# Optimization experiments

Measured on AMD Instinct MI355X. Metric: run time of the kernel, lower is better.

## Reference

```python
import jax, jax.numpy as jnp
import numpy as np
import math

PHI = (1.0 + math.sqrt(5.0)) / 2.0
B, S, E, H = 4, 1024, 1024, 16
D = E // H  # head_dim = 64


def setup_inputs() -> dict:
    key = jax.random.key(0)
    ks = jax.random.split(key, 16)
    w = 0.02  # stand-in for xavier(gain=1/phi); math is init-agnostic
    inp = {
        "query": jax.random.normal(ks[0], (B, S, E), jnp.float32),
        "key": jax.random.normal(ks[1], (B, S, E), jnp.float32),
        "value": jax.random.normal(ks[2], (B, S, E), jnp.float32),
        "consciousness_levels": jax.random.uniform(ks[3], (B, S), jnp.float32),
        # causal mask, broadcast over batch and heads
        "attn_mask": jnp.tril(jnp.ones((S, S), bool))[None, None],
        # projection weights stored [in, out] (torch Linear applies x @ W.T)
        "Wq": jax.random.normal(ks[4], (E, E), jnp.float32) * w,
        "bq": jnp.zeros((E,), jnp.float32),
        "Wk": jax.random.normal(ks[5], (E, E), jnp.float32) * w,
        "bk": jnp.zeros((E,), jnp.float32),
        "Wv": jax.random.normal(ks[6], (E, E), jnp.float32) * w,
        "bv": jnp.zeros((E,), jnp.float32),
        "Wo": jax.random.normal(ks[7], (E, E), jnp.float32) * w,
        "bo": jnp.zeros((E,), jnp.float32),
        "Wc": jax.random.normal(ks[8], (E, H), jnp.float32) * w,
        "bc": jnp.zeros((H,), jnp.float32),
        # phi_bias[h] = (h+1)/phi**(h+1), shape [H,1,1] as in _init_weights
        "phi_bias": jnp.array([(h + 1) / PHI ** (h + 1) for h in range(H)],
                               jnp.float32).reshape(H, 1, 1),
    }
    return inp


def reference(query, key, value, consciousness_levels, attn_mask,
              Wq, bq, Wk, bk, Wv, bv, Wo, bo, Wc, bc, phi_bias):
    # project and split heads: [B,S,E] -> [B,H,S,D]
    q = (query @ Wq + bq).reshape(B, S, H, D).transpose(0, 2, 1, 3)
    k = (key @ Wk + bk).reshape(B, S, H, D).transpose(0, 2, 1, 3)
    v = (value @ Wv + bv).reshape(B, S, H, D).transpose(0, 2, 1, 3)

    inv_scale = 1.0 / (math.sqrt(D) * math.sqrt(PHI))  # phi-scaled 1/sqrt(d)
    scores = jnp.einsum('bhqd,bhkd->bhqk', q, k) * inv_scale
    scores = scores + phi_bias[None]                   # per-head additive bias
    scores = jnp.where(attn_mask, scores, -jnp.inf)
    attn = jax.nn.softmax(scores, axis=-1)             # [B,H,S,S]

    # consciousness reweighting + second softmax (faithful to original)
    cw = jax.nn.softmax(query @ Wc + bc, axis=-1)      # [B,S,H]
    cw = cw.transpose(0, 2, 1)[..., None]              # [B,H,S,1]
    cb = consciousness_levels[:, None, :, None]        # [B,1,S,1]
    attn = jax.nn.softmax(attn * (1.0 + cb * cw), axis=-1)

    ctx = jnp.einsum('bhqk,bhkd->bhqd', attn, v)
    ctx = ctx.transpose(0, 2, 1, 3).reshape(B, S, E)
    out = ctx @ Wo + bo
    return out, attn
```

## Files before the change

kernel.cpp:

```cpp
#include <hip/hip_runtime.h>
#include <stdint.h>

#define B_ 4
#define S_ 1024
#define E_ 1024
#define H_ 16
#define D_ 64

typedef unsigned short u16;
typedef short s16x8 __attribute__((ext_vector_type(8)));
typedef unsigned short u16x8 __attribute__((ext_vector_type(8)));
typedef unsigned short u16x4 __attribute__((ext_vector_type(4)));
typedef unsigned short u16x2 __attribute__((ext_vector_type(2)));
typedef float f32x4 __attribute__((ext_vector_type(4)));

__device__ __forceinline__ u16 f2bf(float f) {
    union { float f; uint32_t i; } x; x.f = f;
    uint32_t r = (x.i + 0x7FFFu + ((x.i >> 16) & 1u)) >> 16;
    return (u16)r;
}

__device__ __forceinline__ float wave_sum(float v) {
    #pragma unroll
    for (int o = 32; o; o >>= 1) v += __shfl_xor(v, o);
    return v;
}

__device__ __forceinline__ void gload16(const u16* g, u16* l) {
    __builtin_amdgcn_global_load_lds(
        (const __attribute__((address_space(1))) void*)g,
        (__attribute__((address_space(3))) void*)l, 16, 0, 0);
}

template<int BM, int BN>
__device__ __forceinline__ void gemm_core(
    const u16* __restrict__ Ab, int lda,
    const u16* __restrict__ Bp, int ldb,
    int m0, int n0, int K,
    u16* As, u16* Bs, f32x4 (&acc)[BM / 32][BN / 32])
{
    constexpr int FM = BM / 32, FN = BN / 32;
    constexpr int ACH = BM / 64;
    constexpr int BCH = BN / 64;
    const int t = threadIdx.x, lane = t & 63, w = t >> 6;
    const int wr = w >> 1, wc = w & 1, al = lane & 15, aq = lane >> 4;

    for (int k0 = 0; k0 < K; k0 += 32) {
        #pragma unroll
        for (int i = 0; i < ACH; i++) {
            const int c = i * 256 + w * 64 + lane;
            gload16(Ab + (size_t)(m0 + (c >> 2)) * lda + k0 + (c & 3) * 8,
                    As + (size_t)(i * 256 + w * 64) * 8);
        }
        #pragma unroll
        for (int i = 0; i < BCH; i++) {
            const int c = i * 256 + w * 64 + lane;
            gload16(Bp + (size_t)(n0 + (c >> 2)) * ldb + k0 + (c & 3) * 8,
                    Bs + (size_t)(i * 256 + w * 64) * 8);
        }
        asm volatile("s_waitcnt vmcnt(0)" ::: "memory");
        __syncthreads();

        s16x8 af[FM], bf[FN];
        #pragma unroll
        for (int i = 0; i < FM; i++)
            af[i] = *(const s16x8*)(As + ((wr * FM + i) * 16 + al) * 32 + aq * 8);
        #pragma unroll
        for (int j = 0; j < FN; j++)
            bf[j] = *(const s16x8*)(Bs + ((wc * FN + j) * 16 + al) * 32 + aq * 8);
        #pragma unroll
        for (int i = 0; i < FM; i++)
            #pragma unroll
            for (int j = 0; j < FN; j++)
                acc[i][j] = __builtin_amdgcn_mfma_f32_16x16x32_bf16(af[i], bf[j], acc[i][j], 0, 0, 0);
        __syncthreads();
    }
}

__global__ __launch_bounds__(256, 3)
void gemm_qkv(const u16* __restrict__ qbf, const u16* __restrict__ kbf,
              const u16* __restrict__ vbf, const u16* __restrict__ wt,
              const float* __restrict__ bq, const float* __restrict__ bk,
              const float* __restrict__ bv,
              u16* __restrict__ q_ws, u16* __restrict__ k_ws,
              u16* __restrict__ vt_ws)
{
    __shared__ __attribute__((aligned(16))) u16 As[128 * 32];
    __shared__ __attribute__((aligned(16))) u16 Bs[128 * 32];
    const int z = blockIdx.z;
    const u16* Ab = (z == 0) ? qbf : (z == 1) ? kbf : vbf;
    const u16* Bp = wt + (size_t)z * E_ * E_;
    const float* bias = (z == 0) ? bq : (z == 1) ? bk : bv;
    u16* Cb = (z == 0) ? q_ws : (z == 1) ? k_ws : vt_ws;
    const int m0 = blockIdx.y * 128, n0 = blockIdx.x * 128;

    f32x4 acc[4][4];
    #pragma unroll
    for (int i = 0; i < 4; i++)
        #pragma unroll
        for (int j = 0; j < 4; j++)
            acc[i][j] = (f32x4){0.f, 0.f, 0.f, 0.f};

    gemm_core<128, 128>(Ab, E_, Bp, E_, m0, n0, E_, As, Bs, acc);

    const int t = threadIdx.x, lane = t & 63, w = t >> 6;
    const int wr = w >> 1, wc = w & 1, al = lane & 15, aq = lane >> 4;
    #pragma unroll
    for (int i = 0; i < 4; i++) {
        #pragma unroll
        for (int j = 0; j < 4; j++) {
            const int col = n0 + (wc * 4 + j) * 16 + al;
            const float bvv = bias[col];
            #pragma unroll
            for (int r = 0; r < 4; r++) {
                const int row = m0 + (wr * 4 + i) * 16 + aq * 4 + r;
                const float vv = acc[i][j][r] + bvv;
                const int b = row >> 10, s = row & 1023, h = col >> 6, d = col & 63;
                if (z < 2)
                    Cb[((size_t)((b * H_ + h) * S_ + s)) * D_ + d] = f2bf(vv);
                else
                    Cb[((size_t)((b * H_ + h) * D_ + d)) * S_ + s] = f2bf(vv);
            }
        }
    }
}

__global__ __launch_bounds__(256, 3)
void gemm_o(const u16* __restrict__ ctx, const u16* __restrict__ wt3,
            const float* __restrict__ bo, float* __restrict__ out)
{
    __shared__ __attribute__((aligned(16))) u16 As[128 * 32];
    __shared__ __attribute__((aligned(16))) u16 Bs[64 * 32];
    const int m0 = blockIdx.y * 128, n0 = blockIdx.x * 64;

    f32x4 acc[4][2];
    #pragma unroll
    for (int i = 0; i < 4; i++)
        #pragma unroll
        for (int j = 0; j < 2; j++)
            acc[i][j] = (f32x4){0.f, 0.f, 0.f, 0.f};

    gemm_core<128, 64>(ctx, E_, wt3, E_, m0, n0, E_, As, Bs, acc);

    const int t = threadIdx.x, lane = t & 63, w = t >> 6;
    const int wr = w >> 1, wc = w & 1, al = lane & 15, aq = lane >> 4;
    #pragma unroll
    for (int i = 0; i < 4; i++) {
        #pragma unroll
        for (int j = 0; j < 2; j++) {
            const int col = n0 + (wc * 2 + j) * 16 + al;
            const float bvv = bo[col];
            #pragma unroll
            for (int r = 0; r < 4; r++) {
                const int row = m0 + (wr * 4 + i) * 16 + aq * 4 + r;
                out[(size_t)row * E_ + col] = acc[i][j][r] + bvv;
            }
        }
    }
}

__device__ __forceinline__ void cvt8(const float* __restrict__ src,
                                     u16* __restrict__ dst, int i) {
    f32x4 a = *(const f32x4*)(src + (size_t)i * 8);
    f32x4 b = *(const f32x4*)(src + (size_t)i * 8 + 4);
    u16x8 o;
    o[0] = f2bf(a[0]); o[1] = f2bf(a[1]); o[2] = f2bf(a[2]); o[3] = f2bf(a[3]);
    o[4] = f2bf(b[0]); o[5] = f2bf(b[1]); o[6] = f2bf(b[2]); o[7] = f2bf(b[3]);
    *(u16x8*)(dst + (size_t)i * 8) = o;
}

__global__ __launch_bounds__(256)
void cvt3_k(const float* __restrict__ q, const float* __restrict__ k,
            const float* __restrict__ v, u16* __restrict__ oq,
            u16* __restrict__ ok, u16* __restrict__ ov)
{
    const int n = B_ * S_ * E_ / 8;
    for (int i = blockIdx.x * 256 + threadIdx.x; i < n; i += gridDim.x * 256) {
        cvt8(q, oq, i);
        cvt8(k, ok, i);
        cvt8(v, ov, i);
    }
}

__global__ __launch_bounds__(256)
void cons_k(const float* __restrict__ query, const float* __restrict__ Wc,
            const float* __restrict__ bc, const float* __restrict__ cl,
            float* __restrict__ mws)
{
    const int t = threadIdx.x, lane = t & 63, wave = t >> 6;
    const int r = blockIdx.x * 4 + wave;
    const float* qrow = query + (size_t)r * E_;
    float acc[H_];
    #pragma unroll
    for (int c = 0; c < H_; c++) acc[c] = 0.f;
    for (int e = lane; e < E_; e += 64) {
        float qv = qrow[e];
        const float* wp = Wc + e * H_;
        f32x4 w0 = *(const f32x4*)(wp);
        f32x4 w1 = *(const f32x4*)(wp + 4);
        f32x4 w2 = *(const f32x4*)(wp + 8);
        f32x4 w3 = *(const f32x4*)(wp + 12);
        #pragma unroll
        for (int c = 0; c < 4; c++) {
            acc[c]      += qv * w0[c];
            acc[4 + c]  += qv * w1[c];
            acc[8 + c]  += qv * w2[c];
            acc[12 + c] += qv * w3[c];
        }
    }
    #pragma unroll
    for (int c = 0; c < H_; c++) acc[c] = wave_sum(acc[c]);
    float mx = -3e38f;
    #pragma unroll
    for (int c = 0; c < H_; c++) { acc[c] += bc[c]; mx = fmaxf(mx, acc[c]); }
    float se = 0.f;
    #pragma unroll
    for (int c = 0; c < H_; c++) { acc[c] = __expf(acc[c] - mx); se += acc[c]; }
    if (lane < H_) {
        float mycw = 0.f;
        #pragma unroll
        for (int c = 0; c < H_; c++) if (lane == c) mycw = acc[c];
        mycw /= se;
        int b = r >> 10, s = r & 1023;
        float clv = cl[r];
        mws[((size_t)(b * H_ + lane)) * S_ + s] = 1.f + clv * mycw;
    }
}

#define LD_ 1028
__global__ __launch_bounds__(512, 4)
void attn_fused(const u16* __restrict__ q_ws, const u16* __restrict__ k_ws,
                const u16* __restrict__ vt_ws, const float* __restrict__ mws,
                float* __restrict__ attn_out, u16* __restrict__ ctx_ws,
                float alpha)
{
    __shared__ __attribute__((aligned(16))) float sc[16 * LD_];
    __shared__ float red[32 * 16];
    __shared__ float rowmax[16], scl1[16], invz[16];

    const int t = threadIdx.x, lane = t & 63, w = t >> 6;
    const int al = lane & 15, aq = lane >> 4;
    const int bh = blockIdx.y;
    const int q0 = blockIdx.x * 16;

    const u16* Qp = q_ws + ((size_t)bh * S_ + q0) * D_;
    const u16* Kp = k_ws + ((size_t)bh * S_ + w * 128) * D_;
    const u16* Vp = vt_ws + (size_t)bh * D_ * S_;

    s16x8 qf0 = *(const s16x8*)(Qp + (size_t)al * D_ + aq * 8);
    s16x8 qf1 = *(const s16x8*)(Qp + (size_t)al * D_ + 32 + aq * 8);
    #pragma unroll
    for (int mf = 0; mf < 8; mf++) {
        const u16* kr = Kp + (size_t)(mf * 16 + al) * D_ + aq * 8;
        s16x8 kf0 = *(const s16x8*)(kr);
        s16x8 kf1 = *(const s16x8*)(kr + 32);
        f32x4 a0 = (f32x4){0.f, 0.f, 0.f, 0.f};
        a0 = __builtin_amdgcn_mfma_f32_16x16x32_bf16(kf0, qf0, a0, 0, 0, 0);
        a0 = __builtin_amdgcn_mfma_f32_16x16x32_bf16(kf1, qf1, a0, 0, 0, 0);
        const int kc = w * 128 + mf * 16 + aq * 4;
        f32x4 o;
        #pragma unroll
        for (int j = 0; j < 4; j++) o[j] = a0[j] * alpha;
        *(f32x4*)(sc + (size_t)al * LD_ + kc) = o;
    }
    __syncthreads();

    const int row = t & 15, cg = t >> 4;
    const int q = q0 + row;
    float* rp = sc + (size_t)row * LD_ + cg * 4;

    f32x4 sv[8];
    float mx = -3e38f;
    #pragma unroll
    for (int k = 0; k < 8; k++) {
        sv[k] = *(const f32x4*)(rp + k * 128);
        const int cb = cg * 4 + k * 128;
        #pragma unroll
        for (int j = 0; j < 4; j++)
            if (cb + j <= q) mx = fmaxf(mx, sv[k][j]);
    }
    red[cg * 16 + row] = mx;
    __syncthreads();
    if (t < 16) {
        float m = red[t];
        #pragma unroll
        for (int c = 1; c < 32; c++) m = fmaxf(m, red[c * 16 + t]);
        rowmax[t] = m;
    }
    __syncthreads();

    const float mxr = rowmax[row];
    float s1 = 0.f;
    #pragma unroll
    for (int k = 0; k < 8; k++) {
        const int cb = cg * 4 + k * 128;
        #pragma unroll
        for (int j = 0; j < 4; j++) {
            float e = (cb + j <= q) ? __expf(sv[k][j] - mxr) : 0.f;
            sv[k][j] = e; s1 += e;
        }
    }
    red[cg * 16 + row] = s1;
    __syncthreads();
    if (t < 16) {
        float s = 0.f;
        #pragma unroll
        for (int c = 0; c < 32; c++) s += red[c * 16 + t];
        scl1[t] = mws[(size_t)bh * S_ + q0 + t] / s;
    }
    __syncthreads();

    const float sl = scl1[row];
    float s2 = 0.f;
    #pragma unroll
    for (int k = 0; k < 8; k++) {
        const int cb = cg * 4 + k * 128;
        f32x4 o;
        #pragma unroll
        for (int j = 0; j < 4; j++) {
            float e = (cb + j <= q) ? __expf(sv[k][j] * sl) : 1.f;
            o[j] = e; s2 += e;
        }
        *(f32x4*)(rp + k * 128) = o;
    }
    red[cg * 16 + row] = s2;
    __syncthreads();
    if (t < 16) {
        float s = 0.f;
        #pragma unroll
        for (int c = 0; c < 32; c++) s += red[c * 16 + t];
        invz[t] = 1.f / s;
    }
    __syncthreads();

    f32x4 pa[4];
    #pragma unroll
    for (int nf = 0; nf < 4; nf++) pa[nf] = (f32x4){0.f, 0.f, 0.f, 0.f};
    #pragma unroll
    for (int ks = 0; ks < 4; ks++) {
        const int kb = w * 128 + ks * 32;
        const float* ap = sc + (size_t)al * LD_ + kb + aq * 8;
        f32x4 x0 = *(const f32x4*)(ap);
        f32x4 x1 = *(const f32x4*)(ap + 4);
        s16x8 af;
        af[0] = (short)f2bf(x0[0]); af[1] = (short)f2bf(x0[1]);
        af[2] = (short)f2bf(x0[2]); af[3] = (short)f2bf(x0[3]);
        af[4] = (short)f2bf(x1[0]); af[5] = (short)f2bf(x1[1]);
        af[6] = (short)f2bf(x1[2]); af[7] = (short)f2bf(x1[3]);
        #pragma unroll
        for (int nf = 0; nf < 4; nf++) {
            s16x8 bfv = *(const s16x8*)(Vp + (size_t)(nf * 16 + al) * S_ + kb + aq * 8);
            pa[nf] = __builtin_amdgcn_mfma_f32_16x16x32_bf16(af, bfv, pa[nf], 0, 0, 0);
        }
    }

    float* ao = attn_out + (size_t)bh * S_ * S_ + (size_t)q0 * S_;
    #pragma unroll
    for (int rr = 0; rr < 2; rr++) {
        const int r2 = w * 2 + rr;
        const float iz = invz[r2];
        #pragma unroll
        for (int k2 = 0; k2 < 4; k2++) {
            f32x4 v = *(const f32x4*)(sc + (size_t)r2 * LD_ + k2 * 256 + lane * 4);
            f32x4 o;
            #pragma unroll
            for (int j = 0; j < 4; j++) o[j] = v[j] * iz;
            *(f32x4*)(ao + (size_t)r2 * S_ + k2 * 256 + lane * 4) = o;
        }
    }
    __syncthreads();

    {
        float* dp = sc + w * (64 * 20);
        #pragma unroll
        for (int nf = 0; nf < 4; nf++)
            *(f32x4*)(dp + (size_t)(nf * 16 + al) * 20 + aq * 4) = pa[nf];
    }
    __syncthreads();
    {
        const int r5 = t >> 5, d0 = (t & 31) * 2;
        const float iz = invz[r5];
        float o0 = 0.f, o1 = 0.f;
        #pragma unroll
        for (int ww = 0; ww < 8; ww++) {
            const float* rp5 = sc + ww * (64 * 20) + r5;
            o0 += rp5[(size_t)d0 * 20];
            o1 += rp5[(size_t)(d0 + 1) * 20];
        }
        const int b = bh >> 4, h = bh & 15;
        u16* cp = ctx_ws + ((size_t)(b * S_ + q0 + r5)) * E_ + h * 64 + d0;
        u16x2 ob;
        ob[0] = f2bf(o0 * iz);
        ob[1] = f2bf(o1 * iz);
        *(u16x2*)cp = ob;
    }
}

__global__ __launch_bounds__(256)
void transpose4_k(const float* __restrict__ W0, const float* __restrict__ W1,
                  const float* __restrict__ W2, const float* __restrict__ W3,
                  u16* __restrict__ out)
{
    __shared__ float tile[32][33];
    const int zz = blockIdx.z;
    const float* in = (zz == 0) ? W0 : (zz == 1) ? W1 : (zz == 2) ? W2 : W3;
    u16* o = out + (size_t)zz * E_ * E_;
    const int t = threadIdx.x;
    const int tx = t & 31, ty = t >> 5;
    const int bx = blockIdx.x * 32, by = blockIdx.y * 32;
    #pragma unroll
    for (int i = 0; i < 32; i += 8)
        tile[ty + i][tx] = in[(size_t)(by + ty + i) * E_ + bx + tx];
    __syncthreads();
    #pragma unroll
    for (int i = 0; i < 32; i += 8)
        o[(size_t)(bx + ty + i) * E_ + by + tx] = f2bf(tile[tx][ty + i]);
}

extern "C" void kernel_launch(void* const* d_in, const int* in_sizes, int n_in,
                              void* d_out, int out_size, void* d_ws, size_t ws_size,
                              hipStream_t stream)
{
    const float* query = (const float*)d_in[0];
    const float* key_  = (const float*)d_in[1];
    const float* value = (const float*)d_in[2];
    const float* cl    = (const float*)d_in[3];
    const float* Wq = (const float*)d_in[5];
    const float* bq = (const float*)d_in[6];
    const float* Wk = (const float*)d_in[7];
    const float* bk = (const float*)d_in[8];
    const float* Wv = (const float*)d_in[9];
    const float* bv = (const float*)d_in[10];
    const float* Wo = (const float*)d_in[11];
    const float* bo = (const float*)d_in[12];
    const float* Wc = (const float*)d_in[13];
    const float* bc = (const float*)d_in[14];

    float* out  = (float*)d_out;
    float* attn = out + (size_t)B_ * S_ * E_;

    u16* q_ws   = (u16*)d_ws;
    u16* k_ws   = q_ws  + (size_t)B_ * S_ * E_;
    u16* vt_ws  = k_ws  + (size_t)B_ * S_ * E_;
    u16* ctx_ws = vt_ws + (size_t)B_ * S_ * E_;
    u16* wt     = ctx_ws + (size_t)B_ * S_ * E_;
    float* mws  = (float*)(wt + (size_t)4 * E_ * E_);

    u16* qbf = (u16*)attn;
    u16* kbf = qbf + (size_t)B_ * S_ * E_;
    u16* vbf = kbf + (size_t)B_ * S_ * E_;

    const float inv_scale = 0.09826892502579689f;
    dim3 blk(256);

    transpose4_k<<<dim3(32, 32, 4), blk, 0, stream>>>(Wq, Wk, Wv, Wo, wt);

    cvt3_k<<<2048, blk, 0, stream>>>(query, key_, value, qbf, kbf, vbf);

    cons_k<<<B_ * S_ / 4, blk, 0, stream>>>(query, Wc, bc, cl, mws);

    gemm_qkv<<<dim3(8, 32, 3), blk, 0, stream>>>(
        qbf, kbf, vbf, wt, bq, bk, bv, q_ws, k_ws, vt_ws);

    attn_fused<<<dim3(S_ / 16, B_ * H_), dim3(512), 0, stream>>>(
        q_ws, k_ws, vt_ws, mws, attn, ctx_ws, inv_scale);

    gemm_o<<<dim3(16, 32, 1), blk, 0, stream>>>(
        ctx_ws, wt + (size_t)3 * E_ * E_, bo, out);
}
```

Baseline: 556.8 us.

## Keep attention scores in registers, stage bf16 probabilities, and swizzle block order

The attention kernel now applies the mask and exponentials straight on the MFMA accumulators and keeps them in registers, instead of round-tripping fp32 scores through a large LDS tile. Row sums use wave shuffles plus a small LDS reduction. The unnormalised probabilities go into LDS as bf16 for the PV MFMA, which shrinks shared memory to raise occupancy. The row-max pass is dropped, which risks overflow if scores get large. All three kernels also remap block indices so neighbouring blocks share operand tiles in cache, and the attn_out stores become narrower per-lane scalar writes.

```diff
diff --git a/kernel.cpp b/kernel.cpp
--- a/kernel.cpp
+++ b/kernel.cpp
@@ -87,12 +87,15 @@
 {
     __shared__ __attribute__((aligned(16))) u16 As[128 * 32];
     __shared__ __attribute__((aligned(16))) u16 Bs[128 * 32];
-    const int z = blockIdx.z;
+    const int flat = blockIdx.x + (blockIdx.y << 3) + (blockIdx.z << 8);
+    const int z = flat >> 8;
+    const int y = flat & 31;
+    const int x = (flat >> 5) & 7;
     const u16* Ab = (z == 0) ? qbf : (z == 1) ? kbf : vbf;
     const u16* Bp = wt + (size_t)z * E_ * E_;
     const float* bias = (z == 0) ? bq : (z == 1) ? bk : bv;
     u16* Cb = (z == 0) ? q_ws : (z == 1) ? k_ws : vt_ws;
-    const int m0 = blockIdx.y * 128, n0 = blockIdx.x * 128;
+    const int m0 = y * 128, n0 = x * 128;
 
     f32x4 acc[4][4];
     #pragma unroll
@@ -131,7 +134,10 @@
 {
     __shared__ __attribute__((aligned(16))) u16 As[128 * 32];
     __shared__ __attribute__((aligned(16))) u16 Bs[64 * 32];
-    const int m0 = blockIdx.y * 128, n0 = blockIdx.x * 64;
+    const int flat = blockIdx.x + (blockIdx.y << 4);
+    const int y = flat & 31;
+    const int x = flat >> 5;
+    const int m0 = y * 128, n0 = x * 64;
 
     f32x4 acc[4][2];
     #pragma unroll
@@ -227,109 +233,114 @@
     }
 }
 
-#define LD_ 1028
+#define LDP 1048
 __global__ __launch_bounds__(512, 4)
 void attn_fused(const u16* __restrict__ q_ws, const u16* __restrict__ k_ws,
                 const u16* __restrict__ vt_ws, const float* __restrict__ mws,
                 float* __restrict__ attn_out, u16* __restrict__ ctx_ws,
                 float alpha)
 {
-    __shared__ __attribute__((aligned(16))) float sc[16 * LD_];
-    __shared__ float red[32 * 16];
-    __shared__ float rowmax[16], scl1[16], invz[16];
+    __shared__ __attribute__((aligned(16))) char shraw[8 * 64 * 20 * 4];
+    u16*   Pl  = (u16*)shraw;
+    float* dmp = (float*)shraw;
+    __shared__ float red[8 * 16];
+    __shared__ float sclA[16], invzA[16];
 
     const int t = threadIdx.x, lane = t & 63, w = t >> 6;
     const int al = lane & 15, aq = lane >> 4;
-    const int bh = blockIdx.y;
-    const int q0 = blockIdx.x * 16;
+    const int flat = blockIdx.x + (blockIdx.y << 6);
+    const int bh = flat & 63;
+    const int q0 = (flat >> 6) << 4;
 
     const u16* Qp = q_ws + ((size_t)bh * S_ + q0) * D_;
     const u16* Kp = k_ws + ((size_t)bh * S_ + w * 128) * D_;
     const u16* Vp = vt_ws + (size_t)bh * D_ * S_;
 
-    s16x8 qf0 = *(const s16x8*)(Qp + (size_t)al * D_ + aq * 8);
-    s16x8 qf1 = *(const s16x8*)(Qp + (size_t)al * D_ + 32 + aq * 8);
+    s16x8 qa0 = *(const s16x8*)(Qp + (size_t)al * D_ + aq * 8);
+    s16x8 qa1 = *(const s16x8*)(Qp + (size_t)al * D_ + 32 + aq * 8);
+    f32x4 ee[8];
+    f32x4 s1 = (f32x4){0.f, 0.f, 0.f, 0.f};
     #pragma unroll
     for (int mf = 0; mf < 8; mf++) {
         const u16* kr = Kp + (size_t)(mf * 16 + al) * D_ + aq * 8;
-        s16x8 kf0 = *(const s16x8*)(kr);
-        s16x8 kf1 = *(const s16x8*)(kr + 32);
+        s16x8 kb0 = *(const s16x8*)(kr);
+        s16x8 kb1 = *(const s16x8*)(kr + 32);
         f32x4 a0 = (f32x4){0.f, 0.f, 0.f, 0.f};
-        a0 = __builtin_amdgcn_mfma_f32_16x16x32_bf16(kf0, qf0, a0, 0, 0, 0);
-        a0 = __builtin_amdgcn_mfma_f32_16x16x32_bf16(kf1, qf1, a0, 0, 0, 0);
-        const int kc = w * 128 + mf * 16 + aq * 4;
-        f32x4 o;
-        #pragma unroll
-        for (int j = 0; j < 4; j++) o[j] = a0[j] * alpha;
-        *(f32x4*)(sc + (size_t)al * LD_ + kc) = o;
-    }
-    __syncthreads();
-
-    const int row = t & 15, cg = t >> 4;
-    const int q = q0 + row;
-    float* rp = sc + (size_t)row * LD_ + cg * 4;
-
-    f32x4 sv[8];
-    float mx = -3e38f;
-    #pragma unroll
-    for (int k = 0; k < 8; k++) {
-        sv[k] = *(const f32x4*)(rp + k * 128);
-        const int cb = cg * 4 + k * 128;
-        #pragma unroll
-        for (int j = 0; j < 4; j++)
-            if (cb + j <= q) mx = fmaxf(mx, sv[k][j]);
-    }
-    red[cg * 16 + row] = mx;
-    __syncthreads();
-    if (t < 16) {
-        float m = red[t];
-        #pragma unroll
-        for (int c = 1; c < 32; c++) m = fmaxf(m, red[c * 16 + t]);
-        rowmax[t] = m;
-    }
-    __syncthreads();
-
-    const float mxr = rowmax[row];
-    float s1 = 0.f;
-    #pragma unroll
-    for (int k = 0; k < 8; k++) {
-        const int cb = cg * 4 + k * 128;
-        #pragma unroll
-        for (int j = 0; j < 4; j++) {
-            float e = (cb + j <= q) ? __expf(sv[k][j] - mxr) : 0.f;
-            sv[k][j] = e; s1 += e;
-        }
-    }
-    red[cg * 16 + row] = s1;
+        a0 = __builtin_amdgcn_mfma_f32_16x16x32_bf16(qa0, kb0, a0, 0, 0, 0);
+        a0 = __builtin_amdgcn_mfma_f32_16x16x32_bf16(qa1, kb1, a0, 0, 0, 0);
+        const int kk = w * 128 + mf * 16 + al;
+        #pragma unroll
+        for (int r = 0; r < 4; r++) {
+            const int qg = q0 + aq * 4 + r;
+            float e = (kk <= qg) ? __expf(a0[r] * alpha) : 0.f;
+            ee[mf][r] = e;
+            s1[r] += e;
+        }
+    }
+    #pragma unroll
+    for (int o = 1; o <= 8; o <<= 1) {
+        #pragma unroll
+        for (int r = 0; r < 4; r++) s1[r] += __shfl_xor(s1[r], o);
+    }
+    if (al == 0) {
+        #pragma unroll
+        for (int r = 0; r < 4; r++) red[w * 16 + aq * 4 + r] = s1[r];
+    }
     __syncthreads();
     if (t < 16) {
         float s = 0.f;
         #pragma unroll
-        for (int c = 0; c < 32; c++) s += red[c * 16 + t];
-        scl1[t] = mws[(size_t)bh * S_ + q0 + t] / s;
-    }
-    __syncthreads();
-
-    const float sl = scl1[row];
-    float s2 = 0.f;
-    #pragma unroll
-    for (int k = 0; k < 8; k++) {
-        const int cb = cg * 4 + k * 128;
-        f32x4 o;
-        #pragma unroll
-        for (int j = 0; j < 4; j++) {
-            float e = (cb + j <= q) ? __expf(sv[k][j] * sl) : 1.f;
-            o[j] = e; s2 += e;
-        }
-        *(f32x4*)(rp + k * 128) = o;
-    }
-    red[cg * 16 + row] = s2;
+        for (int c = 0; c < 8; c++) s += red[c * 16 + t];
+        sclA[t] = mws[(size_t)bh * S_ + q0 + t] / s;
+    }
+    __syncthreads();
+
+    float scl_r[4];
+    #pragma unroll
+    for (int r = 0; r < 4; r++) scl_r[r] = sclA[aq * 4 + r];
+    f32x4 s2 = (f32x4){0.f, 0.f, 0.f, 0.f};
+    #pragma unroll
+    for (int mf = 0; mf < 8; mf++) {
+        const int kk = w * 128 + mf * 16 + al;
+        #pragma unroll
+        for (int r = 0; r < 4; r++) {
+            const int qg = q0 + aq * 4 + r;
+            float e = (kk <= qg) ? __expf(ee[mf][r] * scl_r[r]) : 1.f;
+            ee[mf][r] = e;
+            s2[r] += e;
+        }
+    }
+    #pragma unroll
+    for (int o = 1; o <= 8; o <<= 1) {
+        #pragma unroll
+        for (int r = 0; r < 4; r++) s2[r] += __shfl_xor(s2[r], o);
+    }
+    if (al == 0) {
+        #pragma unroll
+        for (int r = 0; r < 4; r++) red[w * 16 + aq * 4 + r] = s2[r];
+    }
     __syncthreads();
     if (t < 16) {
         float s = 0.f;
         #pragma unroll
-        for (int c = 0; c < 32; c++) s += red[c * 16 + t];
-        invz[t] = 1.f / s;
+        for (int c = 0; c < 8; c++) s += red[c * 16 + t];
+        invzA[t] = 1.f / s;
+    }
+    __syncthreads();
+
+    float iz_r[4];
+    #pragma unroll
+    for (int r = 0; r < 4; r++) iz_r[r] = invzA[aq * 4 + r];
+    float* ao = attn_out + (size_t)bh * S_ * S_ + (size_t)q0 * S_;
+    #pragma unroll
+    for (int mf = 0; mf < 8; mf++) {
+        const int kk = w * 128 + mf * 16 + al;
+        #pragma unroll
+        for (int r = 0; r < 4; r++) {
+            const int rq = aq * 4 + r;
+            ao[(size_t)rq * S_ + kk] = ee[mf][r] * iz_r[r];
+            Pl[(size_t)rq * LDP + kk] = f2bf(ee[mf][r]);
+        }
     }
     __syncthreads();
 
@@ -339,39 +350,17 @@
     #pragma unroll
     for (int ks = 0; ks < 4; ks++) {
         const int kb = w * 128 + ks * 32;
-        const float* ap = sc + (size_t)al * LD_ + kb + aq * 8;
-        f32x4 x0 = *(const f32x4*)(ap);
-        f32x4 x1 = *(const f32x4*)(ap + 4);
-        s16x8 af;
-        af[0] = (short)f2bf(x0[0]); af[1] = (short)f2bf(x0[1]);
-        af[2] = (short)f2bf(x0[2]); af[3] = (short)f2bf(x0[3]);
-        af[4] = (short)f2bf(x1[0]); af[5] = (short)f2bf(x1[1]);
-        af[6] = (short)f2bf(x1[2]); af[7] = (short)f2bf(x1[3]);
+        s16x8 af = *(const s16x8*)(Pl + (size_t)al * LDP + kb + aq * 8);
         #pragma unroll
         for (int nf = 0; nf < 4; nf++) {
-            s16x8 bfv = *(const s16x8*)(Vp + (size_t)(nf * 16 + al) * S_ + kb + aq * 8);
-            pa[nf] = __builtin_amdgcn_mfma_f32_16x16x32_bf16(af, bfv, pa[nf], 0, 0, 0);
-        }
-    }
-
-    float* ao = attn_out + (size_t)bh * S_ * S_ + (size_t)q0 * S_;
-    #pragma unroll
-    for (int rr = 0; rr < 2; rr++) {
-        const int r2 = w * 2 + rr;
-        const float iz = invz[r2];
-        #pragma unroll
-        for (int k2 = 0; k2 < 4; k2++) {
-            f32x4 v = *(const f32x4*)(sc + (size_t)r2 * LD_ + k2 * 256 + lane * 4);
-            f32x4 o;
-            #pragma unroll
-            for (int j = 0; j < 4; j++) o[j] = v[j] * iz;
-            *(f32x4*)(ao + (size_t)r2 * S_ + k2 * 256 + lane * 4) = o;
+            s16x8 bv = *(const s16x8*)(Vp + (size_t)(nf * 16 + al) * S_ + kb + aq * 8);
+            pa[nf] = __builtin_amdgcn_mfma_f32_16x16x32_bf16(af, bv, pa[nf], 0, 0, 0);
         }
     }
     __syncthreads();
 
     {
-        float* dp = sc + w * (64 * 20);
+        float* dp = dmp + w * (64 * 20);
         #pragma unroll
         for (int nf = 0; nf < 4; nf++)
             *(f32x4*)(dp + (size_t)(nf * 16 + al) * 20 + aq * 4) = pa[nf];
@@ -379,11 +368,11 @@
     __syncthreads();
     {
         const int r5 = t >> 5, d0 = (t & 31) * 2;
-        const float iz = invz[r5];
+        const float iz = invzA[r5];
         float o0 = 0.f, o1 = 0.f;
         #pragma unroll
         for (int ww = 0; ww < 8; ww++) {
-            const float* rp5 = sc + ww * (64 * 20) + r5;
+            const float* rp5 = dmp + ww * (64 * 20) + r5;
             o0 += rp5[(size_t)d0 * 20];
             o1 += rp5[(size_t)(d0 + 1) * 20];
         }
```

Measured after the change: 554.2 us. No clear change (-0.5%).
